# Kernel optimization log

Hardware: AMD Instinct MI355X
Metric: run time of the kernel (lower is better)

Reference implementation:

```python
import jax, jax.numpy as jnp
import numpy as np

INPUT_DIM = 256
HIDDEN_DIM = 512
BATCH = 64
SEQ = 512


def setup_inputs() -> dict:
    key = jax.random.key(0)
    k1, k2, k3, k4, k5 = jax.random.split(key, 5)
    s = 1.0 / np.sqrt(HIDDEN_DIM)
    x = jax.random.normal(k1, (BATCH, SEQ, INPUT_DIM), dtype=jnp.float32)
    # PyTorch GRU param layout: [3*H, in] with gate order (r, z, n)
    W_ih = jax.random.uniform(k2, (3 * HIDDEN_DIM, INPUT_DIM), minval=-s, maxval=s, dtype=jnp.float32)
    W_hh = jax.random.uniform(k3, (3 * HIDDEN_DIM, HIDDEN_DIM), minval=-s, maxval=s, dtype=jnp.float32)
    b_ih = jax.random.uniform(k4, (3 * HIDDEN_DIM,), minval=-s, maxval=s, dtype=jnp.float32)
    b_hh = jax.random.uniform(k5, (3 * HIDDEN_DIM,), minval=-s, maxval=s, dtype=jnp.float32)
    return {"x": x, "W_ih": W_ih, "W_hh": W_hh, "b_ih": b_ih, "b_hh": b_hh}


def _gru_last(x, W_ih, W_hh, b_ih, b_hh):
    B, T, _ = x.shape
    H = W_hh.shape[1]
    # Precompute input projections for all timesteps: [B, T, 3H]
    x_proj = jnp.einsum('bti,gi->btg', x, W_ih) + b_ih
    x_proj = jnp.swapaxes(x_proj, 0, 1)  # [T, B, 3H] for scan

    def step(h, xp):
        h_proj = h @ W_hh.T + b_hh  # [B, 3H]
        xr, xz, xn = jnp.split(xp, 3, axis=-1)
        hr, hz, hn = jnp.split(h_proj, 3, axis=-1)
        r = jax.nn.sigmoid(xr + hr)
        z = jax.nn.sigmoid(xz + hz)
        n = jnp.tanh(xn + r * hn)
        h_new = (1.0 - z) * n + z * h
        return h_new, None

    h0 = jnp.zeros((B, H), dtype=x.dtype)
    h_last, _ = jax.lax.scan(step, h0, x_proj)
    return h_last  # equals output[:, -1, :] for unidirectional single-layer GRU


def reference(x, W_ih, W_hh, b_ih, b_hh):
    return _gru_last(x, W_ih, W_hh, b_ih, b_hh)
```

## Files before the change

### kernel.cpp

```cpp
#include <hip/hip_runtime.h>
#include <hip/hip_bf16.h>


#define NB 64
#define NT 512
#define NI 256
#define NH 512

typedef __attribute__((ext_vector_type(8))) short bf16x8;
typedef __attribute__((ext_vector_type(4))) float f32x4;
typedef __attribute__((ext_vector_type(4))) int i32x4;

static __device__ __forceinline__ short f2b(float f) {
  unsigned u = __builtin_bit_cast(unsigned, f);
  unsigned r = (u + 0x7fffu + ((u >> 16) & 1u)) >> 16;
  return (short)r;
}
static __device__ __forceinline__ float sigm(float x) {
  return 1.0f / (1.0f + __expf(-x));
}
static __device__ __forceinline__ float tanh_f(float x) {
  return 1.0f - 2.0f / (__expf(2.0f * x) + 1.0f);
}

__global__ __launch_bounds__(256, 1)
void gru_persistent(const float* __restrict__ x,
                    const float* __restrict__ Wih,
                    const float* __restrict__ Whh,
                    const float* __restrict__ bih,
                    const float* __restrict__ bhh,
                    float* __restrict__ out,
                    unsigned char* __restrict__ ws) {
  const int wg   = blockIdx.x;
  const int tid  = threadIdx.x;
  const int wave = tid >> 6;
  const int lane = tid & 63;
  const int c    = lane & 15;
  const int q    = lane >> 4;

  int* slots = (int*)ws;
  int* tags  = (int*)(ws + 8192);
  unsigned short* hb0 = (unsigned short*)(ws + 16384);
  unsigned short* hb1 = (unsigned short*)(ws + 16384 + 65536);
  unsigned short* xb  = (unsigned short*)(ws + 16384 + 2 * 65536);

  __shared__ unsigned short trans[4][16][8];

  {
    const float4* x4 = (const float4*)x;
    const int total4 = NB * NT * NI / 4;
    const int nthr = NB * 256;
    for (int i = wg * 256 + tid; i < total4; i += nthr) {
      float4 v = x4[i];
      ushort4 o;
      o.x = (unsigned short)f2b(v.x);
      o.y = (unsigned short)f2b(v.y);
      o.z = (unsigned short)f2b(v.z);
      o.w = (unsigned short)f2b(v.w);
      ((ushort4*)xb)[i] = o;
    }
    ((unsigned int*)hb0)[wg * 256 + tid] = 0u;
    if (wg == 0) tags[tid] = 0;
  }

  bf16x8 wh[2][16];
  bf16x8 wi[2][8];
#pragma unroll
  for (int nt = 0; nt < 2; nt++) {
    int nl = nt * 16 + c;
    bool valid = nl < 24;
    int gate = nl >> 3;
    int jj = nl & 7;
    int grow = valid ? (gate * NH + wg * 8 + jj) : 0;
#pragma unroll
    for (int kk = 0; kk < 16; kk++) {
      const float* p = Whh + (size_t)grow * NH + kk * 32 + q * 8;
      bf16x8 f;
#pragma unroll
      for (int e = 0; e < 8; e++) f[e] = valid ? f2b(p[e]) : (short)0;
      wh[nt][kk] = f;
    }
#pragma unroll
    for (int kk = 0; kk < 8; kk++) {
      const float* p = Wih + (size_t)grow * NI + kk * 32 + q * 8;
      bf16x8 f;
#pragma unroll
      for (int e = 0; e < 8; e++) f[e] = valid ? f2b(p[e]) : (short)0;
      wi[nt][kk] = f;
    }
  }

  const int jcol = wg * 8 + (c & 7);
  const float bri = bih[jcol],          brh = bhh[jcol];
  const float bzi = bih[NH + jcol],     bzh = bhh[NH + jcol];
  const float bni = bih[2 * NH + jcol], bnh = bhh[2 * NH + jcol];

  float hold[4] = {0.f, 0.f, 0.f, 0.f};

  __syncthreads();
  if (tid == 0)
    __hip_atomic_store(&slots[wg * 32], 1, __ATOMIC_RELEASE,
                       __HIP_MEMORY_SCOPE_AGENT);
  if (wave == 0) {
    while (__hip_atomic_load(&slots[lane * 32], __ATOMIC_RELAXED,
                             __HIP_MEMORY_SCOPE_AGENT) < 1)
      __builtin_amdgcn_s_sleep(1);
  }
  __syncthreads();
  __threadfence();

  const int b0 = wave * 16 + c;
  int* mytags = tags + wave * 64;
  const int* tagp = mytags + lane;

  for (int t = 0; t < NT; t++) {
    const unsigned short* hcur = (t & 1) ? hb1 : hb0;
    unsigned short* hnext      = (t & 1) ? hb0 : hb1;

    f32x4 aX0 = {0.f, 0.f, 0.f, 0.f}, aX1 = {0.f, 0.f, 0.f, 0.f};
    f32x4 aH0 = {0.f, 0.f, 0.f, 0.f}, aH1 = {0.f, 0.f, 0.f, 0.f};

    const bf16x8* xr = (const bf16x8*)(xb + ((size_t)b0 * NT + t) * NI);

#pragma unroll
    for (int kk = 0; kk < 8; kk++) {
      bf16x8 a = xr[kk * 4 + q];
      aX0 = __builtin_amdgcn_mfma_f32_16x16x32_bf16(a, wi[0][kk], aX0, 0, 0, 0);
      aX1 = __builtin_amdgcn_mfma_f32_16x16x32_bf16(a, wi[1][kk], aX1, 0, 0, 0);
    }

    if (t > 0) {
      const int need = t + 1;
      while (true) {
        int v;
        asm volatile("global_load_dword %0, %1, off sc1"
                     : "=v"(v) : "v"(tagp));
        asm volatile("s_waitcnt vmcnt(0)" : "+v"(v)::"memory");
        if (__all(v >= need)) break;
      }
    }

    i32x4 hv[16];
    {
      const char* hb = (const char*)hcur;
#pragma unroll
      for (int kk = 0; kk < 16; kk++) {
        const void* ap = hb + (size_t)(((kk * 4 + q) * 64 + b0) << 4);
        asm volatile("global_load_dwordx4 %0, %1, off sc1"
                     : "=v"(hv[kk]) : "v"(ap));
      }
      asm volatile("s_waitcnt vmcnt(0)"
                   : "+v"(hv[0]), "+v"(hv[1]), "+v"(hv[2]), "+v"(hv[3]),
                     "+v"(hv[4]), "+v"(hv[5]), "+v"(hv[6]), "+v"(hv[7]),
                     "+v"(hv[8]), "+v"(hv[9]), "+v"(hv[10]), "+v"(hv[11]),
                     "+v"(hv[12]), "+v"(hv[13]), "+v"(hv[14]), "+v"(hv[15])
                   ::"memory");
    }

#pragma unroll
    for (int kk = 0; kk < 16; kk++) {
      bf16x8 a = __builtin_bit_cast(bf16x8, hv[kk]);
      aH0 = __builtin_amdgcn_mfma_f32_16x16x32_bf16(a, wh[0][kk], aH0, 0, 0, 0);
      aH1 = __builtin_amdgcn_mfma_f32_16x16x32_bf16(a, wh[1][kk], aH1, 0, 0, 0);
    }

#pragma unroll
    for (int r = 0; r < 4; r++) {
      float xz = __shfl_xor(aX0[r], 8, 64);
      float hz = __shfl_xor(aH0[r], 8, 64);
      float rr = sigm(aX0[r] + bri + aH0[r] + brh);
      float zz = sigm(xz + bzi + hz + bzh);
      float nn = tanh_f(aX1[r] + bni + rr * (aH1[r] + bnh));
      float hv2 = (1.0f - zz) * nn + zz * hold[r];
      hold[r] = hv2;
      if (c < 8) trans[wave][q * 4 + r][c] = (unsigned short)f2b(hv2);
    }

    if (t < NT - 1) {
      asm volatile("s_waitcnt lgkmcnt(0)" ::: "memory");
      if (lane < 16) {
        int b = wave * 16 + lane;
        const unsigned long long* tp =
            (const unsigned long long*)&trans[wave][lane][0];
        unsigned long long v0 = tp[0], v1 = tp[1];
        unsigned long long* dst =
            (unsigned long long*)(hnext + ((size_t)wg * 64 + b) * 8);
        __hip_atomic_store(dst, v0, __ATOMIC_RELAXED, __HIP_MEMORY_SCOPE_AGENT);
        __hip_atomic_store(dst + 1, v1, __ATOMIC_RELAXED,
                           __HIP_MEMORY_SCOPE_AGENT);
      }
      asm volatile("s_waitcnt vmcnt(0)" ::: "memory");
      if (lane == 0)
        __hip_atomic_store(&mytags[wg], t + 2, __ATOMIC_RELAXED,
                           __HIP_MEMORY_SCOPE_AGENT);
    }
  }

  if (c < 8) {
#pragma unroll
    for (int r = 0; r < 4; r++) {
      int b = wave * 16 + q * 4 + r;
      out[(size_t)b * NH + wg * 8 + c] = hold[r];
    }
  }
}

extern "C" void kernel_launch(void* const* d_in, const int* in_sizes, int n_in,
                              void* d_out, int out_size, void* d_ws, size_t ws_size,
                              hipStream_t stream) {
  const float* x   = (const float*)d_in[0];
  const float* Wih = (const float*)d_in[1];
  const float* Whh = (const float*)d_in[2];
  const float* bih = (const float*)d_in[3];
  const float* bhh = (const float*)d_in[4];
  float* out = (float*)d_out;
  hipLaunchKernelGGL(gru_persistent, dim3(NB), dim3(256), 0, stream,
                     x, Wih, Whh, bih, bhh, out, (unsigned char*)d_ws);
}
```

Baseline: 1.834 ms.

## Embed step tags in hidden-state words to drop per-step flag wait

```diff
diff --git a/kernel.cpp b/kernel.cpp
--- a/kernel.cpp
+++ b/kernel.cpp
@@ -10,6 +10,7 @@
 typedef __attribute__((ext_vector_type(8))) short bf16x8;
 typedef __attribute__((ext_vector_type(4))) float f32x4;
 typedef __attribute__((ext_vector_type(4))) int i32x4;
+typedef __attribute__((ext_vector_type(4))) unsigned int u32x4;
 
 static __device__ __forceinline__ short f2b(float f) {
   unsigned u = __builtin_bit_cast(unsigned, f);
@@ -40,11 +41,11 @@
 
   int* slots = (int*)ws;
   int* tags  = (int*)(ws + 8192);
-  unsigned short* hb0 = (unsigned short*)(ws + 16384);
-  unsigned short* hb1 = (unsigned short*)(ws + 16384 + 65536);
-  unsigned short* xb  = (unsigned short*)(ws + 16384 + 2 * 65536);
-
-  __shared__ unsigned short trans[4][16][8];
+  unsigned* hb0 = (unsigned*)(ws + 16384);
+  unsigned* hb1 = (unsigned*)(ws + 16384 + 131072);
+  unsigned short* xb = (unsigned short*)(ws + 16384 + 262144);
+
+  __shared__ __align__(16) unsigned short trans[4][16][8];
 
   {
     const float4* x4 = (const float4*)x;
@@ -59,8 +60,9 @@
       o.w = (unsigned short)f2b(v.w);
       ((ushort4*)xb)[i] = o;
     }
-    ((unsigned int*)hb0)[wg * 256 + tid] = 0u;
+    for (int i = wg * 256 + tid; i < 65536; i += nthr) hb0[i] = 0u;
     if (wg == 0) tags[tid] = 0;
+    ((unsigned*)trans)[tid] = 0u;
   }
 
   bf16x8 wh[2][16];
@@ -112,10 +114,66 @@
   const int b0 = wave * 16 + c;
   int* mytags = tags + wave * 64;
   const int* tagp = mytags + lane;
+  const int kk_own = wg >> 2;
+  const bool own = (q == (wg & 3));
+
+#define LOAD_ALL()                                                            \
+  do {                                                                        \
+    const char* hbase_ = (const char*)hcur;                                   \
+    _Pragma("unroll") for (int kk2 = 0; kk2 < 16; kk2++) {                    \
+      const void* ap_ = hbase_ + (size_t)(((kk2 * 4 + q) * 64 + b0) << 5);    \
+      asm volatile("global_load_dwordx4 %0, %1, off sc1"                      \
+                   : "=v"(hv[kk2][0]) : "v"(ap_));                            \
+      asm volatile("global_load_dwordx4 %0, %1, off offset:16 sc1"            \
+                   : "=v"(hv[kk2][1]) : "v"(ap_));                            \
+    }                                                                         \
+  } while (0)
+
+#define WAIT_ALL()                                                            \
+  do {                                                                        \
+    asm volatile("s_waitcnt vmcnt(0)"                                         \
+        : "+v"(hv[0][0]), "+v"(hv[0][1]), "+v"(hv[1][0]), "+v"(hv[1][1]),     \
+          "+v"(hv[2][0]), "+v"(hv[2][1]), "+v"(hv[3][0]), "+v"(hv[3][1]),     \
+          "+v"(hv[4][0]), "+v"(hv[4][1]), "+v"(hv[5][0]), "+v"(hv[5][1]),     \
+          "+v"(hv[6][0]), "+v"(hv[6][1]), "+v"(hv[7][0]), "+v"(hv[7][1])      \
+        :: "memory");                                                         \
+    asm volatile("s_waitcnt vmcnt(0)"                                         \
+        : "+v"(hv[8][0]),  "+v"(hv[8][1]),  "+v"(hv[9][0]),  "+v"(hv[9][1]),  \
+          "+v"(hv[10][0]), "+v"(hv[10][1]), "+v"(hv[11][0]), "+v"(hv[11][1]), \
+          "+v"(hv[12][0]), "+v"(hv[12][1]), "+v"(hv[13][0]), "+v"(hv[13][1]), \
+          "+v"(hv[14][0]), "+v"(hv[14][1]), "+v"(hv[15][0]), "+v"(hv[15][1]), \
+          "+v"(tv)                                                            \
+        :: "memory");                                                         \
+  } while (0)
+
+#define SUBVAL(mn_)                                                           \
+  do {                                                                        \
+    _Pragma("unroll") for (int kk2 = 0; kk2 < 16; kk2++) {                    \
+      if (kk2 == kk_own) {                                                    \
+        hv[kk2][0][0] = own ? (int)td0 : hv[kk2][0][0];                       \
+        hv[kk2][0][1] = own ? (int)td1 : hv[kk2][0][1];                       \
+        hv[kk2][0][2] = own ? (int)td2 : hv[kk2][0][2];                       \
+        hv[kk2][0][3] = own ? (int)td3 : hv[kk2][0][3];                       \
+        hv[kk2][1][0] = own ? (int)td4 : hv[kk2][1][0];                       \
+        hv[kk2][1][1] = own ? (int)td5 : hv[kk2][1][1];                       \
+        hv[kk2][1][2] = own ? (int)td6 : hv[kk2][1][2];                       \
+        hv[kk2][1][3] = own ? (int)td7 : hv[kk2][1][3];                       \
+      }                                                                       \
+    }                                                                         \
+    mn_ = 0xffffffffu;                                                        \
+    _Pragma("unroll") for (int kk2 = 0; kk2 < 16; kk2++) {                    \
+      _Pragma("unroll") for (int h2 = 0; h2 < 2; h2++) {                      \
+        _Pragma("unroll") for (int j2 = 0; j2 < 4; j2++) {                    \
+          unsigned d_ = (unsigned)hv[kk2][h2][j2];                            \
+          mn_ = d_ < mn_ ? d_ : mn_;                                          \
+        }                                                                     \
+      }                                                                       \
+    }                                                                         \
+  } while (0)
 
   for (int t = 0; t < NT; t++) {
-    const unsigned short* hcur = (t & 1) ? hb1 : hb0;
-    unsigned short* hnext      = (t & 1) ? hb0 : hb1;
+    const unsigned* hcur = (t & 1) ? hb1 : hb0;
+    unsigned* hnext      = (t & 1) ? hb0 : hb1;
 
     f32x4 aX0 = {0.f, 0.f, 0.f, 0.f}, aX1 = {0.f, 0.f, 0.f, 0.f};
     f32x4 aH0 = {0.f, 0.f, 0.f, 0.f}, aH1 = {0.f, 0.f, 0.f, 0.f};
@@ -129,37 +187,54 @@
       aX1 = __builtin_amdgcn_mfma_f32_16x16x32_bf16(a, wi[1][kk], aX1, 0, 0, 0);
     }
 
-    if (t > 0) {
-      const int need = t + 1;
+    const unsigned bound = (unsigned)t << 16;
+
+    i32x4 hv[16][2];
+    int tv = t;
+
+    LOAD_ALL();
+    if (t > 0)
+      asm volatile("global_load_dword %0, %1, off sc1" : "=v"(tv) : "v"(tagp));
+
+    const unsigned* lp = (const unsigned*)&trans[wave][c][0];
+    unsigned lw0 = lp[0], lw1 = lp[1], lw2 = lp[2], lw3 = lp[3];
+    unsigned td0 = bound | (lw0 & 0xffffu), td1 = bound | (lw0 >> 16);
+    unsigned td2 = bound | (lw1 & 0xffffu), td3 = bound | (lw1 >> 16);
+    unsigned td4 = bound | (lw2 & 0xffffu), td5 = bound | (lw2 >> 16);
+    unsigned td6 = bound | (lw3 & 0xffffu), td7 = bound | (lw3 >> 16);
+
+    WAIT_ALL();
+    unsigned mn;
+    SUBVAL(mn);
+    bool data_ok = __all((int)(mn >= bound));
+
+    if (t > 0 && !data_ok) {
       while (true) {
         int v;
-        asm volatile("global_load_dword %0, %1, off sc1"
-                     : "=v"(v) : "v"(tagp));
+        asm volatile("global_load_dword %0, %1, off sc1" : "=v"(v) : "v"(tagp));
         asm volatile("s_waitcnt vmcnt(0)" : "+v"(v)::"memory");
-        if (__all(v >= need)) break;
+        if (__all(v >= t)) break;
       }
     }
-
-    i32x4 hv[16];
-    {
-      const char* hb = (const char*)hcur;
-#pragma unroll
-      for (int kk = 0; kk < 16; kk++) {
-        const void* ap = hb + (size_t)(((kk * 4 + q) * 64 + b0) << 4);
-        asm volatile("global_load_dwordx4 %0, %1, off sc1"
-                     : "=v"(hv[kk]) : "v"(ap));
-      }
-      asm volatile("s_waitcnt vmcnt(0)"
-                   : "+v"(hv[0]), "+v"(hv[1]), "+v"(hv[2]), "+v"(hv[3]),
-                     "+v"(hv[4]), "+v"(hv[5]), "+v"(hv[6]), "+v"(hv[7]),
-                     "+v"(hv[8]), "+v"(hv[9]), "+v"(hv[10]), "+v"(hv[11]),
-                     "+v"(hv[12]), "+v"(hv[13]), "+v"(hv[14]), "+v"(hv[15])
-                   ::"memory");
+    while (!data_ok) {
+      LOAD_ALL();
+      WAIT_ALL();
+      SUBVAL(mn);
+      data_ok = __all((int)(mn >= bound));
     }
 
 #pragma unroll
     for (int kk = 0; kk < 16; kk++) {
-      bf16x8 a = __builtin_bit_cast(bf16x8, hv[kk]);
+      unsigned w0 = __builtin_amdgcn_perm((unsigned)hv[kk][0][1],
+                                          (unsigned)hv[kk][0][0], 0x05040100u);
+      unsigned w1 = __builtin_amdgcn_perm((unsigned)hv[kk][0][3],
+                                          (unsigned)hv[kk][0][2], 0x05040100u);
+      unsigned w2 = __builtin_amdgcn_perm((unsigned)hv[kk][1][1],
+                                          (unsigned)hv[kk][1][0], 0x05040100u);
+      unsigned w3 = __builtin_amdgcn_perm((unsigned)hv[kk][1][3],
+                                          (unsigned)hv[kk][1][2], 0x05040100u);
+      u32x4 pk = {w0, w1, w2, w3};
+      bf16x8 a = __builtin_bit_cast(bf16x8, pk);
       aH0 = __builtin_amdgcn_mfma_f32_16x16x32_bf16(a, wh[0][kk], aH0, 0, 0, 0);
       aH1 = __builtin_amdgcn_mfma_f32_16x16x32_bf16(a, wh[1][kk], aH1, 0, 0, 0);
     }
@@ -180,18 +255,22 @@
       asm volatile("s_waitcnt lgkmcnt(0)" ::: "memory");
       if (lane < 16) {
         int b = wave * 16 + lane;
-        const unsigned long long* tp =
-            (const unsigned long long*)&trans[wave][lane][0];
-        unsigned long long v0 = tp[0], v1 = tp[1];
-        unsigned long long* dst =
-            (unsigned long long*)(hnext + ((size_t)wg * 64 + b) * 8);
-        __hip_atomic_store(dst, v0, __ATOMIC_RELAXED, __HIP_MEMORY_SCOPE_AGENT);
-        __hip_atomic_store(dst + 1, v1, __ATOMIC_RELAXED,
-                           __HIP_MEMORY_SCOPE_AGENT);
+        const unsigned* tp = (const unsigned*)&trans[wave][lane][0];
+        unsigned s0 = tp[0], s1 = tp[1], s2 = tp[2], s3 = tp[3];
+        unsigned tg = (unsigned)(t + 1) << 16;
+        i32x4 lo, hi;
+        lo[0] = (int)(tg | (s0 & 0xffffu)); lo[1] = (int)(tg | (s0 >> 16));
+        lo[2] = (int)(tg | (s1 & 0xffffu)); lo[3] = (int)(tg | (s1 >> 16));
+        hi[0] = (int)(tg | (s2 & 0xffffu)); hi[1] = (int)(tg | (s2 >> 16));
+        hi[2] = (int)(tg | (s3 & 0xffffu)); hi[3] = (int)(tg | (s3 >> 16));
+        void* dst = (char*)hnext + ((size_t)(wg * 64 + b) << 5);
+        asm volatile("global_store_dwordx4 %0, %1, off sc1"
+                     :: "v"(dst), "v"(lo) : "memory");
+        asm volatile("global_store_dwordx4 %0, %1, off offset:16 sc1"
+                     :: "v"(dst), "v"(hi) : "memory");
       }
-      asm volatile("s_waitcnt vmcnt(0)" ::: "memory");
       if (lane == 0)
-        __hip_atomic_store(&mytags[wg], t + 2, __ATOMIC_RELAXED,
+        __hip_atomic_store(&mytags[wg], t + 1, __ATOMIC_RELAXED,
                            __HIP_MEMORY_SCOPE_AGENT);
     }
   }
```

After: 2.801 ms. 52.7% more time.

## Publish step tags before stores complete and validate hidden-state loads with sentinels

Applied to the files above, without the earlier changes.

```diff
diff --git a/kernel.cpp b/kernel.cpp
--- a/kernel.cpp
+++ b/kernel.cpp
@@ -6,6 +6,8 @@
 #define NT 512
 #define NI 256
 #define NH 512
+
+#define SENT 0xffffffffu
 
 typedef __attribute__((ext_vector_type(8))) short bf16x8;
 typedef __attribute__((ext_vector_type(4))) float f32x4;
@@ -44,7 +46,7 @@
   unsigned short* hb1 = (unsigned short*)(ws + 16384 + 65536);
   unsigned short* xb  = (unsigned short*)(ws + 16384 + 2 * 65536);
 
-  __shared__ unsigned short trans[4][16][8];
+  __shared__ __align__(16) unsigned short trans[4][16][8];
 
   {
     const float4* x4 = (const float4*)x;
@@ -113,6 +115,36 @@
   int* mytags = tags + wave * 64;
   const int* tagp = mytags + lane;
 
+#define LOAD_ALL()                                                            \
+  do {                                                                        \
+    const char* hbase_ = (const char*)hcur;                                   \
+    _Pragma("unroll") for (int kk2 = 0; kk2 < 16; kk2++) {                    \
+      const void* ap_ = hbase_ + (size_t)(((kk2 * 4 + q) * 64 + b0) << 4);    \
+      asm volatile("global_load_dwordx4 %0, %1, off sc1"                      \
+                   : "=v"(hv[kk2]) : "v"(ap_));                               \
+    }                                                                         \
+  } while (0)
+
+#define WAIT_ALL()                                                            \
+  asm volatile("s_waitcnt vmcnt(0)"                                           \
+               : "+v"(hv[0]), "+v"(hv[1]), "+v"(hv[2]), "+v"(hv[3]),          \
+                 "+v"(hv[4]), "+v"(hv[5]), "+v"(hv[6]), "+v"(hv[7]),          \
+                 "+v"(hv[8]), "+v"(hv[9]), "+v"(hv[10]), "+v"(hv[11]),        \
+                 "+v"(hv[12]), "+v"(hv[13]), "+v"(hv[14]), "+v"(hv[15]),      \
+                 "+v"(va), "+v"(vb)                                           \
+               ::"memory")
+
+#define UMAX64(mx_)                                                           \
+  do {                                                                        \
+    mx_ = 0u;                                                                 \
+    _Pragma("unroll") for (int kk2 = 0; kk2 < 16; kk2++) {                    \
+      _Pragma("unroll") for (int j2 = 0; j2 < 4; j2++) {                      \
+        unsigned d_ = (unsigned)hv[kk2][j2];                                  \
+        mx_ = d_ > mx_ ? d_ : mx_;                                            \
+      }                                                                       \
+    }                                                                         \
+  } while (0)
+
   for (int t = 0; t < NT; t++) {
     const unsigned short* hcur = (t & 1) ? hb1 : hb0;
     unsigned short* hnext      = (t & 1) ? hb0 : hb1;
@@ -129,32 +161,36 @@
       aX1 = __builtin_amdgcn_mfma_f32_16x16x32_bf16(a, wi[1][kk], aX1, 0, 0, 0);
     }
 
+    int va = 0, vb = 0;
+
     if (t > 0) {
       const int need = t + 1;
-      while (true) {
-        int v;
-        asm volatile("global_load_dword %0, %1, off sc1"
-                     : "=v"(v) : "v"(tagp));
-        asm volatile("s_waitcnt vmcnt(0)" : "+v"(v)::"memory");
-        if (__all(v >= need)) break;
+      asm volatile("global_load_dword %0, %1, off sc1" : "=v"(va) : "v"(tagp));
+      for (;;) {
+        asm volatile("global_load_dword %0, %1, off sc1" : "=v"(vb) : "v"(tagp));
+        asm volatile("s_waitcnt vmcnt(1)" : "+v"(va)::"memory");
+        if (__all(va >= need)) break;
+        asm volatile("global_load_dword %0, %1, off sc1" : "=v"(va) : "v"(tagp));
+        asm volatile("s_waitcnt vmcnt(1)" : "+v"(vb)::"memory");
+        if (__all(vb >= need)) break;
       }
     }
 
+    if (t < NT - 1) {
+      unsigned* sp = (unsigned*)hnext + ((wg * 64 + wave * 16) << 2) + lane;
+      asm volatile("global_store_dword %0, %1, off sc1"
+                   :: "v"(sp), "v"(SENT) : "memory");
+    }
+
     i32x4 hv[16];
-    {
-      const char* hb = (const char*)hcur;
-#pragma unroll
-      for (int kk = 0; kk < 16; kk++) {
-        const void* ap = hb + (size_t)(((kk * 4 + q) * 64 + b0) << 4);
-        asm volatile("global_load_dwordx4 %0, %1, off sc1"
-                     : "=v"(hv[kk]) : "v"(ap));
-      }
-      asm volatile("s_waitcnt vmcnt(0)"
-                   : "+v"(hv[0]), "+v"(hv[1]), "+v"(hv[2]), "+v"(hv[3]),
-                     "+v"(hv[4]), "+v"(hv[5]), "+v"(hv[6]), "+v"(hv[7]),
-                     "+v"(hv[8]), "+v"(hv[9]), "+v"(hv[10]), "+v"(hv[11]),
-                     "+v"(hv[12]), "+v"(hv[13]), "+v"(hv[14]), "+v"(hv[15])
-                   ::"memory");
+    LOAD_ALL();
+    WAIT_ALL();
+    unsigned mx;
+    UMAX64(mx);
+    while (!__all((int)(mx != SENT))) {
+      LOAD_ALL();
+      WAIT_ALL();
+      UMAX64(mx);
     }
 
 #pragma unroll
@@ -178,18 +214,14 @@
 
     if (t < NT - 1) {
       asm volatile("s_waitcnt lgkmcnt(0)" ::: "memory");
+      asm volatile("s_waitcnt vmcnt(0)" ::: "memory");
       if (lane < 16) {
         int b = wave * 16 + lane;
-        const unsigned long long* tp =
-            (const unsigned long long*)&trans[wave][lane][0];
-        unsigned long long v0 = tp[0], v1 = tp[1];
-        unsigned long long* dst =
-            (unsigned long long*)(hnext + ((size_t)wg * 64 + b) * 8);
-        __hip_atomic_store(dst, v0, __ATOMIC_RELAXED, __HIP_MEMORY_SCOPE_AGENT);
-        __hip_atomic_store(dst + 1, v1, __ATOMIC_RELAXED,
-                           __HIP_MEMORY_SCOPE_AGENT);
+        i32x4 pk = *(const i32x4*)&trans[wave][lane][0];
+        void* dst = (char*)hnext + ((size_t)(wg * 64 + b) << 4);
+        asm volatile("global_store_dwordx4 %0, %1, off sc1"
+                     :: "v"(dst), "v"(pk) : "memory");
       }
-      asm volatile("s_waitcnt vmcnt(0)" ::: "memory");
       if (lane == 0)
         __hip_atomic_store(&mytags[wg], t + 2, __ATOMIC_RELAXED,
                            __HIP_MEMORY_SCOPE_AGENT);
```

After: 1.921 ms. 1.05x slower.

## Replace flag polling with tagged hidden-state ring and inline x conversion

Applied to the files above, without the earlier changes.

```diff
diff --git a/kernel.cpp b/kernel.cpp
--- a/kernel.cpp
+++ b/kernel.cpp
@@ -10,6 +10,7 @@
 typedef __attribute__((ext_vector_type(8))) short bf16x8;
 typedef __attribute__((ext_vector_type(4))) float f32x4;
 typedef __attribute__((ext_vector_type(4))) int i32x4;
+typedef __attribute__((ext_vector_type(4))) unsigned u32x4;
 
 static __device__ __forceinline__ short f2b(float f) {
   unsigned u = __builtin_bit_cast(unsigned, f);
@@ -38,30 +39,18 @@
   const int c    = lane & 15;
   const int q    = lane >> 4;
 
-  int* slots = (int*)ws;
-  int* tags  = (int*)(ws + 8192);
-  unsigned short* hb0 = (unsigned short*)(ws + 16384);
-  unsigned short* hb1 = (unsigned short*)(ws + 16384 + 65536);
-  unsigned short* xb  = (unsigned short*)(ws + 16384 + 2 * 65536);
-
-  __shared__ unsigned short trans[4][16][8];
-
-  {
-    const float4* x4 = (const float4*)x;
-    const int total4 = NB * NT * NI / 4;
-    const int nthr = NB * 256;
-    for (int i = wg * 256 + tid; i < total4; i += nthr) {
-      float4 v = x4[i];
-      ushort4 o;
-      o.x = (unsigned short)f2b(v.x);
-      o.y = (unsigned short)f2b(v.y);
-      o.z = (unsigned short)f2b(v.z);
-      o.w = (unsigned short)f2b(v.w);
-      ((ushort4*)xb)[i] = o;
-    }
-    ((unsigned int*)hb0)[wg * 256 + tid] = 0u;
-    if (wg == 0) tags[tid] = 0;
-  }
+  unsigned long long* flags = (unsigned long long*)ws;
+  int* prog = (int*)(ws + 4096);
+  int* tags = (int*)(ws + 8192);
+  unsigned short* ringC = (unsigned short*)(ws + 16384);
+  unsigned*       ringT = (unsigned*)(ws + 16384 + 262144);
+
+  __shared__ __align__(16) unsigned short trans[4][16][8];
+
+  const unsigned long long t0 = __builtin_amdgcn_s_memrealtime();
+
+  ((unsigned*)ringC)[wg * 256 + tid] = 0u;
+  if (wg == 0) { tags[tid] = 0; prog[tid] = 0; }
 
   bf16x8 wh[2][16];
   bf16x8 wi[2][8];
@@ -99,69 +88,184 @@
 
   __syncthreads();
   if (tid == 0)
-    __hip_atomic_store(&slots[wg * 32], 1, __ATOMIC_RELEASE,
-                       __HIP_MEMORY_SCOPE_AGENT);
+    __hip_atomic_store(&flags[wg * 8], __builtin_amdgcn_s_memrealtime(),
+                       __ATOMIC_RELEASE, __HIP_MEMORY_SCOPE_AGENT);
   if (wave == 0) {
-    while (__hip_atomic_load(&slots[lane * 32], __ATOMIC_RELAXED,
-                             __HIP_MEMORY_SCOPE_AGENT) < 1)
+    while (__hip_atomic_load(&flags[lane * 8], __ATOMIC_RELAXED,
+                             __HIP_MEMORY_SCOPE_AGENT) < t0)
       __builtin_amdgcn_s_sleep(1);
   }
   __syncthreads();
   __threadfence();
 
+  const unsigned long long f0 =
+      __hip_atomic_load(&flags[0], __ATOMIC_RELAXED, __HIP_MEMORY_SCOPE_AGENT);
+  const unsigned epoch = (unsigned)((f0 >> 14) & 0x7Full);
+
   const int b0 = wave * 16 + c;
+  int* myprog = prog + wave * 64;
   int* mytags = tags + wave * 64;
-  const int* tagp = mytags + lane;
+  const int* tagp  = mytags + lane;
+  const int* progp = myprog + lane;
+
+  const int kk_own = wg >> 2;
+  const bool own   = (q == (wg & 3));
+
+  bool fastMode = true;
+  int  streak   = 0;
 
   for (int t = 0; t < NT; t++) {
-    const unsigned short* hcur = (t & 1) ? hb1 : hb0;
-    unsigned short* hnext      = (t & 1) ? hb0 : hb1;
-
-    f32x4 aX0 = {0.f, 0.f, 0.f, 0.f}, aX1 = {0.f, 0.f, 0.f, 0.f};
-    f32x4 aH0 = {0.f, 0.f, 0.f, 0.f}, aH1 = {0.f, 0.f, 0.f, 0.f};
-
-    const bf16x8* xr = (const bf16x8*)(xb + ((size_t)b0 * NT + t) * NI);
-
+    const int slot = t & 3, nslot = (t + 1) & 3;
+    const unsigned short* rc = ringC + (size_t)slot * 32768;
+    const unsigned*       rt = ringT + (size_t)slot * 32768;
+    unsigned short* rcn = ringC + (size_t)nslot * 32768;
+    unsigned*       rtn = ringT + (size_t)nslot * 32768;
+
+    f32x4 aX0 = {0.f,0.f,0.f,0.f}, aX1 = {0.f,0.f,0.f,0.f};
+    f32x4 aH0 = {0.f,0.f,0.f,0.f}, aH1 = {0.f,0.f,0.f,0.f};
+
+    const float* xrow = x + ((size_t)b0 * NT + t) * NI;
 #pragma unroll
     for (int kk = 0; kk < 8; kk++) {
-      bf16x8 a = xr[kk * 4 + q];
+      const float4* xp = (const float4*)(xrow + kk * 32 + q * 8);
+      float4 u0 = xp[0], u1 = xp[1];
+      unsigned d0, d1, d2, d3;
+      asm("v_cvt_pk_bf16_f32 %0, %1, %2" : "=v"(d0) : "v"(u0.x), "v"(u0.y));
+      asm("v_cvt_pk_bf16_f32 %0, %1, %2" : "=v"(d1) : "v"(u0.z), "v"(u0.w));
+      asm("v_cvt_pk_bf16_f32 %0, %1, %2" : "=v"(d2) : "v"(u1.x), "v"(u1.y));
+      asm("v_cvt_pk_bf16_f32 %0, %1, %2" : "=v"(d3) : "v"(u1.z), "v"(u1.w));
+      u32x4 pk = {d0, d1, d2, d3};
+      bf16x8 a = __builtin_bit_cast(bf16x8, pk);
       aX0 = __builtin_amdgcn_mfma_f32_16x16x32_bf16(a, wi[0][kk], aX0, 0, 0, 0);
       aX1 = __builtin_amdgcn_mfma_f32_16x16x32_bf16(a, wi[1][kk], aX1, 0, 0, 0);
     }
 
-    if (t > 0) {
-      const int need = t + 1;
-      while (true) {
-        int v;
-        asm volatile("global_load_dword %0, %1, off sc1"
-                     : "=v"(v) : "v"(tagp));
-        asm volatile("s_waitcnt vmcnt(0)" : "+v"(v)::"memory");
-        if (__all(v >= need)) break;
-      }
-    }
-
-    i32x4 hv[16];
-    {
-      const char* hb = (const char*)hcur;
+    int pv = 0;
+    if (t < NT - 1)
+      asm volatile("global_load_dword %0, %1, off sc1" : "=v"(pv) : "v"(progp));
+
+    bool done = false;
+
+    if (t > 0 && fastMode) {
+      asm volatile("buffer_inv sc0" ::: "memory");
+      i32x4 hv[16][2];
 #pragma unroll
       for (int kk = 0; kk < 16; kk++) {
-        const void* ap = hb + (size_t)(((kk * 4 + q) * 64 + b0) << 4);
+        const void* ap = (const char*)rt + (size_t)(((kk*4+q)*64 + b0) << 5);
+        asm volatile("global_load_dwordx4 %0, %1, off"
+                     : "=v"(hv[kk][0]) : "v"(ap));
+        asm volatile("global_load_dwordx4 %0, %1, off offset:16"
+                     : "=v"(hv[kk][1]) : "v"(ap));
+      }
+      asm volatile("s_waitcnt vmcnt(0)"
+          : "+v"(hv[0][0]), "+v"(hv[0][1]), "+v"(hv[1][0]), "+v"(hv[1][1]),
+            "+v"(hv[2][0]), "+v"(hv[2][1]), "+v"(hv[3][0]), "+v"(hv[3][1]),
+            "+v"(hv[4][0]), "+v"(hv[4][1]), "+v"(hv[5][0]), "+v"(hv[5][1]),
+            "+v"(hv[6][0]), "+v"(hv[6][1]), "+v"(hv[7][0]), "+v"(hv[7][1])
+          :: "memory");
+      asm volatile("s_waitcnt vmcnt(0)"
+          : "+v"(hv[8][0]),  "+v"(hv[8][1]),  "+v"(hv[9][0]),  "+v"(hv[9][1]),
+            "+v"(hv[10][0]), "+v"(hv[10][1]), "+v"(hv[11][0]), "+v"(hv[11][1]),
+            "+v"(hv[12][0]), "+v"(hv[12][1]), "+v"(hv[13][0]), "+v"(hv[13][1]),
+            "+v"(hv[14][0]), "+v"(hv[14][1]), "+v"(hv[15][0]), "+v"(hv[15][1]),
+            "+v"(pv)
+          :: "memory");
+
+      const unsigned want   = (epoch << 9) | (unsigned)t;
+      const unsigned wanthi = want << 16;
+
+      const unsigned* lp = (const unsigned*)&trans[wave][c][0];
+      unsigned lw0 = lp[0], lw1 = lp[1], lw2 = lp[2], lw3 = lp[3];
+      unsigned td0 = wanthi | (lw0 & 0xffffu), td1 = wanthi | (lw0 >> 16);
+      unsigned td2 = wanthi | (lw1 & 0xffffu), td3 = wanthi | (lw1 >> 16);
+      unsigned td4 = wanthi | (lw2 & 0xffffu), td5 = wanthi | (lw2 >> 16);
+      unsigned td6 = wanthi | (lw3 & 0xffffu), td7 = wanthi | (lw3 >> 16);
+#pragma unroll
+      for (int kk = 0; kk < 16; kk++) {
+        if (kk == kk_own) {
+          hv[kk][0][0] = own ? (int)td0 : hv[kk][0][0];
+          hv[kk][0][1] = own ? (int)td1 : hv[kk][0][1];
+          hv[kk][0][2] = own ? (int)td2 : hv[kk][0][2];
+          hv[kk][0][3] = own ? (int)td3 : hv[kk][0][3];
+          hv[kk][1][0] = own ? (int)td4 : hv[kk][1][0];
+          hv[kk][1][1] = own ? (int)td5 : hv[kk][1][1];
+          hv[kk][1][2] = own ? (int)td6 : hv[kk][1][2];
+          hv[kk][1][3] = own ? (int)td7 : hv[kk][1][3];
+        }
+      }
+      unsigned acc = 0;
+#pragma unroll
+      for (int kk = 0; kk < 16; kk++)
+#pragma unroll
+        for (int h2 = 0; h2 < 2; h2++)
+#pragma unroll
+          for (int j2 = 0; j2 < 4; j2++)
+            acc |= ((unsigned)hv[kk][h2][j2] >> 16) ^ want;
+
+      if (__all((int)(acc == 0))) {
+        streak = 0;
+        if (lane == 0) {
+          int* pp = myprog + wg; int v2 = t + 1;
+          asm volatile("global_store_dword %0, %1, off sc1"
+                       :: "v"(pp), "v"(v2) : "memory");
+        }
+#pragma unroll
+        for (int kk = 0; kk < 16; kk++) {
+          unsigned w0 = __builtin_amdgcn_perm((unsigned)hv[kk][0][1],
+                                              (unsigned)hv[kk][0][0], 0x05040100u);
+          unsigned w1 = __builtin_amdgcn_perm((unsigned)hv[kk][0][3],
+                                              (unsigned)hv[kk][0][2], 0x05040100u);
+          unsigned w2 = __builtin_amdgcn_perm((unsigned)hv[kk][1][1],
+                                              (unsigned)hv[kk][1][0], 0x05040100u);
+          unsigned w3 = __builtin_amdgcn_perm((unsigned)hv[kk][1][3],
+                                              (unsigned)hv[kk][1][2], 0x05040100u);
+          u32x4 pk2 = {w0, w1, w2, w3};
+          bf16x8 a = __builtin_bit_cast(bf16x8, pk2);
+          aH0 = __builtin_amdgcn_mfma_f32_16x16x32_bf16(a, wh[0][kk], aH0, 0,0,0);
+          aH1 = __builtin_amdgcn_mfma_f32_16x16x32_bf16(a, wh[1][kk], aH1, 0,0,0);
+        }
+        done = true;
+      } else {
+        if (++streak >= 4) fastMode = false;
+      }
+    }
+
+    if (!done) {
+      if (t > 0) {
+        const int need = t + 1;
+        for (;;) {
+          int v;
+          asm volatile("global_load_dword %0, %1, off sc1"
+                       : "=v"(v) : "v"(tagp));
+          asm volatile("s_waitcnt vmcnt(0)" : "+v"(v), "+v"(pv) :: "memory");
+          if (__all(v >= need)) break;
+        }
+      }
+      i32x4 hc[16];
+#pragma unroll
+      for (int kk = 0; kk < 16; kk++) {
+        const void* ap = (const char*)rc + (size_t)(((kk*4+q)*64 + b0) << 4);
         asm volatile("global_load_dwordx4 %0, %1, off sc1"
-                     : "=v"(hv[kk]) : "v"(ap));
+                     : "=v"(hc[kk]) : "v"(ap));
       }
       asm volatile("s_waitcnt vmcnt(0)"
-                   : "+v"(hv[0]), "+v"(hv[1]), "+v"(hv[2]), "+v"(hv[3]),
-                     "+v"(hv[4]), "+v"(hv[5]), "+v"(hv[6]), "+v"(hv[7]),
-                     "+v"(hv[8]), "+v"(hv[9]), "+v"(hv[10]), "+v"(hv[11]),
-                     "+v"(hv[12]), "+v"(hv[13]), "+v"(hv[14]), "+v"(hv[15])
-                   ::"memory");
-    }
-
-#pragma unroll
-    for (int kk = 0; kk < 16; kk++) {
-      bf16x8 a = __builtin_bit_cast(bf16x8, hv[kk]);
-      aH0 = __builtin_amdgcn_mfma_f32_16x16x32_bf16(a, wh[0][kk], aH0, 0, 0, 0);
-      aH1 = __builtin_amdgcn_mfma_f32_16x16x32_bf16(a, wh[1][kk], aH1, 0, 0, 0);
+          : "+v"(hc[0]), "+v"(hc[1]), "+v"(hc[2]), "+v"(hc[3]),
+            "+v"(hc[4]), "+v"(hc[5]), "+v"(hc[6]), "+v"(hc[7]),
+            "+v"(hc[8]), "+v"(hc[9]), "+v"(hc[10]), "+v"(hc[11]),
+            "+v"(hc[12]), "+v"(hc[13]), "+v"(hc[14]), "+v"(hc[15]),
+            "+v"(pv)
+          :: "memory");
+      if (lane == 0) {
+        int* pp = myprog + wg; int v2 = t + 1;
+        asm volatile("global_store_dword %0, %1, off sc1"
+                     :: "v"(pp), "v"(v2) : "memory");
+      }
+#pragma unroll
+      for (int kk = 0; kk < 16; kk++) {
+        bf16x8 a = __builtin_bit_cast(bf16x8, hc[kk]);
+        aH0 = __builtin_amdgcn_mfma_f32_16x16x32_bf16(a, wh[0][kk], aH0, 0,0,0);
+        aH1 = __builtin_amdgcn_mfma_f32_16x16x32_bf16(a, wh[1][kk], aH1, 0,0,0);
+      }
     }
 
 #pragma unroll
@@ -177,22 +281,41 @@
     }
 
     if (t < NT - 1) {
+      {
+        const int need = t - 2;
+        while (!__all(pv >= need)) {
+          asm volatile("global_load_dword %0, %1, off sc1"
+                       : "=v"(pv) : "v"(progp));
+          asm volatile("s_waitcnt vmcnt(0)" : "+v"(pv) :: "memory");
+        }
+      }
       asm volatile("s_waitcnt lgkmcnt(0)" ::: "memory");
       if (lane < 16) {
         int b = wave * 16 + lane;
-        const unsigned long long* tp =
-            (const unsigned long long*)&trans[wave][lane][0];
-        unsigned long long v0 = tp[0], v1 = tp[1];
-        unsigned long long* dst =
-            (unsigned long long*)(hnext + ((size_t)wg * 64 + b) * 8);
-        __hip_atomic_store(dst, v0, __ATOMIC_RELAXED, __HIP_MEMORY_SCOPE_AGENT);
-        __hip_atomic_store(dst + 1, v1, __ATOMIC_RELAXED,
-                           __HIP_MEMORY_SCOPE_AGENT);
+        const unsigned* tp = (const unsigned*)&trans[wave][lane][0];
+        unsigned s0 = tp[0], s1 = tp[1], s2 = tp[2], s3 = tp[3];
+        i32x4 pk = *(const i32x4*)tp;
+        void* dc = (char*)rcn + ((size_t)(wg * 64 + b) << 4);
+        asm volatile("global_store_dwordx4 %0, %1, off sc1"
+                     :: "v"(dc), "v"(pk) : "memory");
+        unsigned tg = (((epoch << 9) | (unsigned)(t + 1)) << 16);
+        i32x4 lo, hi;
+        lo[0] = (int)(tg | (s0 & 0xffffu)); lo[1] = (int)(tg | (s0 >> 16));
+        lo[2] = (int)(tg | (s1 & 0xffffu)); lo[3] = (int)(tg | (s1 >> 16));
+        hi[0] = (int)(tg | (s2 & 0xffffu)); hi[1] = (int)(tg | (s2 >> 16));
+        hi[2] = (int)(tg | (s3 & 0xffffu)); hi[3] = (int)(tg | (s3 >> 16));
+        void* dt = (char*)rtn + ((size_t)(wg * 64 + b) << 5);
+        asm volatile("global_store_dwordx4 %0, %1, off sc1"
+                     :: "v"(dt), "v"(lo) : "memory");
+        asm volatile("global_store_dwordx4 %0, %1, off offset:16 sc1"
+                     :: "v"(dt), "v"(hi) : "memory");
       }
       asm volatile("s_waitcnt vmcnt(0)" ::: "memory");
-      if (lane == 0)
-        __hip_atomic_store(&mytags[wg], t + 2, __ATOMIC_RELAXED,
-                           __HIP_MEMORY_SCOPE_AGENT);
+      if (lane == 0) {
+        int* tp2 = mytags + wg; int tv2 = t + 2;
+        asm volatile("global_store_dword %0, %1, off sc1"
+                     :: "v"(tp2), "v"(tv2) : "memory");
+      }
     }
   }
 
```

Result: slower. 3.523 ms (+92.0%).
